# Performance work log

Hardware: AMD Instinct MI355X
Metric: run time of the kernel (lower is better)

The kernel has to match this reference:

```python
import jax, jax.numpy as jnp
import numpy as np

N_BUILDINGS = 4096
NUM_CLUSTERS = 128
EMBED_DIM = 128
TEMPORAL_DIM = 24


def setup_inputs() -> dict:
    key = jax.random.key(0)
    ks = jax.random.split(key, 12)
    E, N, C, T = EMBED_DIM, N_BUILDINGS, NUM_CLUSTERS, TEMPORAL_DIM

    def lin(k, fi, fo):
        k1, k2 = jax.random.split(k)
        w = jax.random.normal(k1, (fo, fi), jnp.float32) / np.sqrt(fi).astype(np.float32)
        b = jax.random.normal(k2, (fo,), jnp.float32) * 0.01
        return w, b

    fp_w1, fp_b1 = lin(ks[0], 2 * E + 2, 128)
    fp_w2, fp_b2 = lin(ks[1], 128, 64)
    fp_w3, fp_b3 = lin(ks[2], 64, 1)
    en_w1, en_b1 = lin(ks[3], 1, 16)
    en_w2, en_b2 = lin(ks[4], 16, 1)
    ps_w1, ps_b1 = lin(ks[5], E, 32)
    ps_w2, ps_b2 = lin(ks[6], 32, 1)

    embeddings = jax.random.normal(ks[7], (1, N, E), jnp.float32)
    generation = jax.random.uniform(ks[8], (1, N, T), jnp.float32) * 50.0
    consumption = jax.random.uniform(ks[9], (1, N, T), jnp.float32) * 50.0
    positions = jax.random.uniform(ks[10], (1, N, 2), jnp.float32) * 1000.0
    cluster_assignments = (jnp.arange(N) % C)[None, :].astype(jnp.int32)

    return dict(embeddings=embeddings, generation=generation, consumption=consumption,
                positions=positions,
                fp_w1=fp_w1, fp_b1=fp_b1, fp_w2=fp_w2, fp_b2=fp_b2, fp_w3=fp_w3, fp_b3=fp_b3,
                en_w1=en_w1, en_b1=en_b1, en_w2=en_w2, en_b2=en_b2,
                ps_w1=ps_w1, ps_b1=ps_b1, ps_w2=ps_w2, ps_b2=ps_b2,
                cluster_assignments=cluster_assignments, num_clusters=C, current_hour=12)


def _greedy_cluster(net0, prio, effm, pf):
    """Greedy allocation within one cluster. net0,prio: [K]; effm,pf: [K,K].
    Surplus rows and deficit cols are both visited in descending priority order;
    non-surplus rows have avail=0 and non-deficit cols have needed<=0, matching the
    original code's subset selection + break/continue semantics."""
    K = net0.shape[0]
    order = jnp.argsort(-prio)
    inv = jnp.argsort(order)
    net_o = net0[order]
    eff_o = effm[order][:, order]
    pf_o = pf[order][:, order]

    def outer(dnet, i):
        avail0 = jnp.maximum(net_o[i], 0.0)  # surplus net is never mutated

        def inner(carry, j):
            avail, dn = carry
            needed = -dn[j]
            active = (avail > 0.0) & (needed > 0.0)
            f = jnp.where(active, jnp.minimum(jnp.minimum(avail, needed), pf_o[i, j]), 0.0)
            dn = dn.at[j].add(f * eff_o[i, j])  # deficit receives delivered flow
            return (avail - f, dn), (f, active)

        (_, dnet), (frow, arow) = jax.lax.scan(inner, (avail0, dnet), jnp.arange(K))
        return dnet, (frow, arow)

    dnet, (flows_o, act_o) = jax.lax.scan(outer, net_o, jnp.arange(K))
    return flows_o[inv][:, inv], act_o[inv][:, inv], dnet[inv]


def _forward(embeddings, generation, consumption, positions,
             fp_w1, fp_b1, fp_w2, fp_b2, fp_w3, fp_b3,
             en_w1, en_b1, en_w2, en_b2,
             ps_w1, ps_b1, ps_w2, ps_b2,
             cluster_assignments, num_clusters, current_hour):
    B, N, E = embeddings.shape
    C = num_clusters
    K = N // C
    net = generation[0, :, current_hour] - consumption[0, :, current_hour]  # [N]

    g = jnp.argsort(cluster_assignments[0]).reshape(C, K)  # [C,K] building ids per cluster
    emb_c = embeddings[0][g]   # [C,K,E]
    pos_c = positions[0][g]    # [C,K,2]
    net_c = net[g]             # [C,K]

    # priority scorer (eval mode)
    h = jax.nn.relu(emb_c @ ps_w1.T + ps_b1)
    prio_c = jax.nn.sigmoid(h @ ps_w2.T + ps_b2)[..., 0]  # [C,K]

    # pairwise distances within cluster
    dist = jnp.linalg.norm(pos_c[:, :, None, :] - pos_c[:, None, :, :], axis=-1)  # [C,K,K]

    # efficiency net: eff = 0.85 + 0.13*sigmoid(MLP(dist/1000))
    eh = jax.nn.relu((dist / 1000.0)[..., None] * en_w1[:, 0] + en_b1)  # [C,K,K,16]
    eff = 0.85 + 0.13 * jax.nn.sigmoid(eh @ en_w2.T + en_b2)[..., 0]    # [C,K,K]

    # flow predictor on concat([emb_i, emb_j, dist, hour/24]); split W1 to avoid
    # materializing the [C,K,K,2E+2] feature tensor. Dropout is eval-mode identity.
    W1a, W1b = fp_w1[:, :E], fp_w1[:, E:2 * E]
    w1d, w1h = fp_w1[:, 2 * E], fp_w1[:, 2 * E + 1]
    hi = emb_c @ W1a.T  # [C,K,128]
    hj = emb_c @ W1b.T  # [C,K,128]
    hour_f = current_hour / 24.0
    h1 = jax.nn.relu(hi[:, :, None, :] + hj[:, None, :, :] + dist[..., None] * w1d + hour_f * w1h + fp_b1)
    h2 = jax.nn.relu(h1 @ fp_w2.T + fp_b2)
    pflow = jax.nn.softplus(h2 @ fp_w3.T + fp_b3)[..., 0]  # [C,K,K]

    flows_c, act_c, dnet_c = jax.vmap(_greedy_cluster)(net_c, prio_c, eff, pflow)

    sharing = jnp.zeros((N, N), embeddings.dtype).at[g[:, :, None], g[:, None, :]].set(flows_c)
    effmat = jnp.ones((N, N), embeddings.dtype).at[g[:, :, None], g[:, None, :]].set(
        jnp.where(act_c, eff, 1.0))
    net_after = jnp.zeros((N,), embeddings.dtype).at[g].set(dnet_c)

    sharing = sharing[None]
    effmat = effmat[None]
    total_shared = sharing.sum()
    energy_sent = sharing.sum(axis=2)
    energy_received = (sharing * effmat).sum(axis=1)
    return sharing, effmat, total_shared, energy_sent, energy_received, net_after[None]


def reference(embeddings, generation, consumption, positions,
              fp_w1, fp_b1, fp_w2, fp_b2, fp_w3, fp_b3,
              en_w1, en_b1, en_w2, en_b2,
              ps_w1, ps_b1, ps_w2, ps_b2,
              cluster_assignments, num_clusters, current_hour):
    return _forward(embeddings, generation, consumption, positions,
                    fp_w1, fp_b1, fp_w2, fp_b2, fp_w3, fp_b3,
                    en_w1, en_b1, en_w2, en_b2,
                    ps_w1, ps_b1, ps_w2, ps_b2,
                    cluster_assignments, num_clusters, current_hour)
```

## Files before the change

kernel.cpp:

```cpp
#include <hip/hip_runtime.h>
#include <math.h>

#define NB 4096
#define NC 128
#define NK 32
#define NE 128

typedef __bf16 bf16x8 __attribute__((ext_vector_type(8)));
typedef float floatx4 __attribute__((ext_vector_type(4)));

__device__ __forceinline__ float sigmoidf_(float x){
  if (x >= 0.f){ float z = expf(-x); return 1.f/(1.f+z); }
  float z = expf(x); return z/(1.f+z);
}
__device__ __forceinline__ float softplusf_(float x){
  return fmaxf(x, 0.f) + log1pf(expf(-fabsf(x)));
}
__device__ __forceinline__ unsigned int pack_bf16(float a, float b){
  unsigned short ua = __builtin_bit_cast(unsigned short, (__bf16)a);
  unsigned short ub = __builtin_bit_cast(unsigned short, (__bf16)b);
  return (unsigned int)ua | ((unsigned int)ub << 16);
}

__global__ void k_hijprio(const float* __restrict__ emb, const float* __restrict__ gen,
                          const float* __restrict__ cons, const float* __restrict__ fp_w1,
                          const float* __restrict__ fp_b1, const float* __restrict__ fp_w2,
                          const float* __restrict__ ps_w1, const float* __restrict__ ps_b1,
                          const float* __restrict__ ps_w2, const float* __restrict__ ps_b2,
                          const int* __restrict__ assign, const int* __restrict__ hourp,
                          float* __restrict__ hi, float* __restrict__ hj,
                          float* __restrict__ net, float* __restrict__ prio,
                          int* __restrict__ g, int* __restrict__ row_of,
                          float* __restrict__ w1d_c, float* __restrict__ bzc,
                          uint4* __restrict__ w2f, float* __restrict__ total){
  int bid = blockIdx.x;
  int t = threadIdx.x;
  if (bid < 512){
    __shared__ float es[8*132];
    __shared__ float wsm[32*132];
    __shared__ float wa_s[128*36];
    __shared__ float wb_s[128*36];
    int i0 = bid*8;
    for (int idx = t; idx < 8*128; idx += 256){
      int b = idx >> 7, e = idx & 127;
      es[b*132 + e] = emb[(i0 + b)*128 + e];
    }
    for (int idx = t; idx < 4096; idx += 256){
      int q = idx >> 7, e = idx & 127;
      wsm[q*132 + e] = ps_w1[q*128 + e];
    }
    int o = t & 127, half = t >> 7;
    float ai[4], aj[4];
#pragma unroll
    for (int r = 0; r < 4; ++r){ ai[r] = 0.f; aj[r] = 0.f; }
    for (int ch = 0; ch < 4; ++ch){
      int ec = ch << 5;
      if (ch) __syncthreads();
      for (int idx = t; idx < 4096; idx += 256){
        int row = idx >> 5, e2 = idx & 31;
        wa_s[row*36 + e2] = fp_w1[row*258 + ec + e2];
        wb_s[row*36 + e2] = fp_w1[row*258 + 128 + ec + e2];
      }
      __syncthreads();
      const float* war = &wa_s[o*36];
      const float* wbr = &wb_s[o*36];
#pragma unroll
      for (int e2 = 0; e2 < 32; e2 += 4){
        float4 wav = *(const float4*)&war[e2];
        float4 wbv = *(const float4*)&wbr[e2];
        float wa0 = wav.x, wa1 = wav.y, wa2 = wav.z, wa3 = wav.w;
        float wb0 = wbv.x, wb1 = wbv.y, wb2 = wbv.z, wb3 = wbv.w;
        int e = ec + e2;
#pragma unroll
        for (int r = 0; r < 4; ++r){
          float4 ev = *(const float4*)&es[(half*4 + r)*132 + e];
          ai[r] = fmaf(ev.x, wa0, fmaf(ev.y, wa1, fmaf(ev.z, wa2, fmaf(ev.w, wa3, ai[r]))));
          aj[r] = fmaf(ev.x, wb0, fmaf(ev.y, wb1, fmaf(ev.z, wb2, fmaf(ev.w, wb3, aj[r]))));
        }
      }
    }
#pragma unroll
    for (int r = 0; r < 4; ++r){
      int b = i0 + half*4 + r;
      hi[b*128 + o] = ai[r];
      hj[b*128 + o] = aj[r];
    }
    {
      int bl = t >> 5, q = t & 31;
      int i = i0 + bl;
      float acc = ps_b1[q];
      const float* er = &es[bl*132];
      const float* wr = &wsm[q*132];
      for (int e = 0; e < 128; e += 4){
        float4 ev = *(const float4*)&er[e];
        float4 wv = *(const float4*)&wr[e];
        acc = fmaf(ev.x, wv.x, acc);
        acc = fmaf(ev.y, wv.y, acc);
        acc = fmaf(ev.z, wv.z, acc);
        acc = fmaf(ev.w, wv.w, acc);
      }
      float v = fmaxf(acc, 0.f) * ps_w2[q];
      for (int m = 16; m >= 1; m >>= 1) v += __shfl_xor(v, m, 32);
      if (q == 0){
        prio[i] = sigmoidf_(v + ps_b2[0]);
        int h = hourp[0];
        net[i] = gen[i*24 + h] - cons[i*24 + h];
      }
    }
  } else if (bid < 528){
    __shared__ int hist[NC];
    __shared__ int loc[256];
    int start = (bid - 512)*256;
    for (int c = t; c < NC; c += 256) hist[c] = 0;
    __syncthreads();
    for (int j = t; j < start; j += 256) atomicAdd(&hist[assign[j]], 1);
    int i = start + t;
    int c = assign[i];
    loc[t] = c;
    __syncthreads();
    int r = hist[c];
    for (int j = 0; j < 256; ++j) r += (j < t && loc[j] == c) ? 1 : 0;
    if (r >= NK) r = NK - 1;
    g[c*NK + r] = i;
    row_of[i] = c*NK + r;
  } else if (bid == 528){
    if (t < 128){
      float hour_f = (float)hourp[0] / 24.0f;
      w1d_c[t] = fp_w1[t*258 + 256];
      bzc[t]   = fmaf(hour_f, fp_w1[t*258 + 257], fp_b1[t]);
    }
    if (t == 128) total[0] = 0.f;
  } else {
    for (int ff = t; ff < 1024; ff += 256){
      int lane = ff & 63, fi = ff >> 6;
      int nt = fi >> 2, ks = fi & 3;
      int o = nt*16 + (lane & 15);
      int kb = ks*32 + (lane >> 4)*8;
      const float* src = fp_w2 + o*128 + kb;
      uint4 u;
      u.x = pack_bf16(src[0], src[1]);
      u.y = pack_bf16(src[2], src[3]);
      u.z = pack_bf16(src[4], src[5]);
      u.w = pack_bf16(src[6], src[7]);
      w2f[ff] = u;
    }
  }
}

__global__ __launch_bounds__(512) void k_pflow(
    const float* __restrict__ hi, const float* __restrict__ hj,
    const float* __restrict__ pos, const float* __restrict__ w1d_c,
    const float* __restrict__ bzc, const uint4* __restrict__ w2f,
    const float* __restrict__ fp_b2, const float* __restrict__ fp_w3,
    const float* __restrict__ fp_b3, const float* __restrict__ en_w1,
    const float* __restrict__ en_b1, const float* __restrict__ en_w2,
    const float* __restrict__ en_b2, const int* __restrict__ g,
    float* __restrict__ pf_g, float* __restrict__ ef_g){
  __shared__ float px[32], py[32];
  __shared__ int gl[32];
  int t = threadIdx.x;
  int lane = t & 63, wv = t >> 6;
  int c = blockIdx.x >> 1, hb = blockIdx.x & 1;
  if (t < 32){
    int b = g[c*NK + t];
    gl[t] = b;
    px[t] = pos[2*b];
    py[t] = pos[2*b + 1];
  }
  __syncthreads();
  {
    int l16 = lane & 15, quad = lane >> 4;
    bf16x8 bfr[4][4];
#pragma unroll
    for (int nt = 0; nt < 4; ++nt)
#pragma unroll
      for (int ks = 0; ks < 4; ++ks)
        bfr[nt][ks] = __builtin_bit_cast(bf16x8, w2f[(nt*4 + ks)*64 + lane]);
    float b2v[4], w3v[4];
#pragma unroll
    for (int nt = 0; nt < 4; ++nt){
      b2v[nt] = fp_b2[nt*16 + l16];
      w3v[nt] = fp_w3[nt*16 + l16];
    }
    float b3 = fp_b3[0];
    const float4* wd4 = (const float4*)w1d_c;
    const float4* bz4 = (const float4*)bzc;
    for (int it = 0; it < 4; ++it){
      int tile = hb*32 + it*8 + wv;
      int i = tile >> 1, j0 = (tile & 1)*16;
      int j = j0 + l16;
      float dx = px[i] - px[j], dy = py[i] - py[j];
      float d = sqrtf(fmaf(dx, dx, dy*dy));
      const float4* hi4 = (const float4*)(hi + gl[i]*128);
      const float4* hj4 = (const float4*)(hj + gl[j]*128);
      bf16x8 af[4];
#pragma unroll
      for (int ks = 0; ks < 4; ++ks){
        int q8 = ks*8 + quad*2;
        float4 a0 = hi4[q8], a1 = hi4[q8 + 1];
        float4 b0 = hj4[q8], b1 = hj4[q8 + 1];
        float4 w0 = wd4[q8], w1 = wd4[q8 + 1];
        float4 z0 = bz4[q8], z1 = bz4[q8 + 1];
        float v0 = fmaxf(a0.x + b0.x + fmaf(d, w0.x, z0.x), 0.f);
        float v1 = fmaxf(a0.y + b0.y + fmaf(d, w0.y, z0.y), 0.f);
        float v2 = fmaxf(a0.z + b0.z + fmaf(d, w0.z, z0.z), 0.f);
        float v3 = fmaxf(a0.w + b0.w + fmaf(d, w0.w, z0.w), 0.f);
        float v4 = fmaxf(a1.x + b1.x + fmaf(d, w1.x, z1.x), 0.f);
        float v5 = fmaxf(a1.y + b1.y + fmaf(d, w1.y, z1.y), 0.f);
        float v6 = fmaxf(a1.z + b1.z + fmaf(d, w1.z, z1.z), 0.f);
        float v7 = fmaxf(a1.w + b1.w + fmaf(d, w1.w, z1.w), 0.f);
        uint4 u;
        u.x = pack_bf16(v0, v1);
        u.y = pack_bf16(v2, v3);
        u.z = pack_bf16(v4, v5);
        u.w = pack_bf16(v6, v7);
        af[ks] = __builtin_bit_cast(bf16x8, u);
      }
      floatx4 acc[4];
#pragma unroll
      for (int nt = 0; nt < 4; ++nt){
        acc[nt] = (floatx4){0.f, 0.f, 0.f, 0.f};
#pragma unroll
        for (int ks = 0; ks < 4; ++ks)
          acc[nt] = __builtin_amdgcn_mfma_f32_16x16x32_bf16(af[ks], bfr[nt][ks], acc[nt], 0, 0, 0);
      }
#pragma unroll
      for (int r = 0; r < 4; ++r){
        float s = 0.f;
#pragma unroll
        for (int nt = 0; nt < 4; ++nt)
          s = fmaf(fmaxf(acc[nt][r] + b2v[nt], 0.f), w3v[nt], s);
#pragma unroll
        for (int m = 8; m >= 1; m >>= 1) s += __shfl_xor(s, m);
        if (l16 == 0)
          pf_g[c*1024 + i*32 + j0 + quad*4 + r] = softplusf_(s + b3);
      }
    }
  }
  {
    int e = hb*512 + t;
    int ii = e >> 5, jj = e & 31;
    float dx = px[ii] - px[jj], dy = py[ii] - py[jj];
    float d = sqrtf(fmaf(dx, dx, dy*dy));
    float ds = d * (1.0f/1000.0f);
    float acc = en_b2[0];
#pragma unroll
    for (int q = 0; q < 16; ++q)
      acc = fmaf(fmaxf(fmaf(ds, en_w1[q], en_b1[q]), 0.f), en_w2[q], acc);
    ef_g[c*1024 + e] = 0.85f + 0.13f*sigmoidf_(acc);
  }
}

__global__ __launch_bounds__(256) void k_gw(
    const float* __restrict__ net, const float* __restrict__ prio,
    const int* __restrict__ g, const float* __restrict__ pf_g,
    const float* __restrict__ ef_g, float* __restrict__ total,
    float* __restrict__ esent, float* __restrict__ erecv, float* __restrict__ nafter,
    float* __restrict__ sharing, float* __restrict__ effm){
  __shared__ float pf_s[1024];
  __shared__ float ef_s[1024];
  __shared__ float fl_s[1024];
  __shared__ float efa_s[1024];
  __shared__ int   mtbl[NB];
  __shared__ int   gl[32];
  __shared__ int   order_s[32];
  int t = threadIdx.x;
  int c = blockIdx.x >> 1, hb = blockIdx.x & 1;
  if (t < 32) gl[t] = g[c*NK + t];
  ((float4*)pf_s)[t] = ((const float4*)(pf_g + c*1024))[t];
  ((float4*)ef_s)[t] = ((const float4*)(ef_g + c*1024))[t];
#pragma unroll
  for (int q = 0; q < 16; ++q) mtbl[q*256 + t] = -1;
  __syncthreads();
  if (t < 32) mtbl[gl[t]] = t;
  if (t < 64){
    int tl = t & 31;
    float pr = (t < 32) ? prio[gl[t]] : -1e30f;
    int rank = 0;
    for (int k = 0; k < 32; ++k){
      float pk = __shfl(pr, k, 32);
      rank += ((pk > pr) || (pk == pr && k < tl)) ? 1 : 0;
    }
    if (t < 32) order_s[rank] = t;
  }
  __syncthreads();
  if (t < 64){
    int tl = t & 31;
    int b = order_s[tl];
    float net0 = net[gl[b]];
    float dnet = net0;
    float recv = 0.f;
    for (int i = 0; i < 32; ++i){
      int a = order_s[i];
      float av0 = fmaxf(__shfl(net0, i, 32), 0.f);
      float pf = pf_s[a*32 + b];
      float ef = ef_s[a*32 + b];
      float needed = -dnet;
      float m = (needed > 0.f) ? fminf(needed, pf) : 0.f;
      float s = m;
#pragma unroll
      for (int dd = 1; dd < 32; dd <<= 1){
        float u = __shfl_up(s, dd, 32);
        if (tl >= dd) s += u;
      }
      float Se = __shfl_up(s, 1, 32);
      if (tl == 0) Se = 0.f;
      float rprev = fmaxf(av0 - Se, 0.f);
      int act = (rprev > 0.f) && (needed > 0.f);
      float f = fminf(m, rprev);
      dnet = fmaf(f, ef, dnet);
      recv = fmaf(f, ef, recv);
      if (t < 32){
        fl_s[a*32 + b]  = f;
        efa_s[a*32 + b] = act ? ef : 1.0f;
      }
    }
    if (hb == 0 && t < 32){
      nafter[gl[b]] = dnet;
      erecv[gl[b]]  = recv;
    }
  }
  __syncthreads();
  if (hb == 0 && t < 32){
    float rs = 0.f;
#pragma unroll
    for (int j = 0; j < 32; ++j)
      rs += fl_s[t*32 + ((j + t) & 31)];
    esent[gl[t]] = rs;
    float cs = rs;
    for (int m = 16; m >= 1; m >>= 1) cs += __shfl_xor(cs, m, 32);
    if (t == 0) atomicAdd(total, cs);
  }
  int mjq[16];
#pragma unroll
  for (int q = 0; q < 4; ++q)
#pragma unroll
    for (int x = 0; x < 4; ++x)
      mjq[q*4 + x] = mtbl[q*1024 + t*4 + x];
  for (int al = 0; al < 16; ++al){
    int a = hb*16 + al;
    long row = (long)gl[a] * NB;
    const float* flr = &fl_s[a*32];
    const float* efr = &efa_s[a*32];
    floatx4* gs = (floatx4*)(sharing + row);
    floatx4* ge = (floatx4*)(effm + row);
#pragma unroll
    for (int q = 0; q < 4; ++q){
      floatx4 vs = (floatx4){0.f, 0.f, 0.f, 0.f};
      floatx4 ve = (floatx4){1.f, 1.f, 1.f, 1.f};
#pragma unroll
      for (int x = 0; x < 4; ++x){
        int mj = mjq[q*4 + x];
        if (mj >= 0){ vs[x] = flr[mj]; ve[x] = efr[mj]; }
      }
      __builtin_nontemporal_store(vs, &gs[q*256 + t]);
      __builtin_nontemporal_store(ve, &ge[q*256 + t]);
    }
  }
}

extern "C" void kernel_launch(void* const* d_in, const int* in_sizes, int n_in,
                              void* d_out, int out_size, void* d_ws, size_t ws_size,
                              hipStream_t stream){
  (void)in_sizes; (void)n_in; (void)out_size; (void)ws_size;
  const float* emb   = (const float*)d_in[0];
  const float* gen   = (const float*)d_in[1];
  const float* cons  = (const float*)d_in[2];
  const float* pos   = (const float*)d_in[3];
  const float* fp_w1 = (const float*)d_in[4];
  const float* fp_b1 = (const float*)d_in[5];
  const float* fp_w2 = (const float*)d_in[6];
  const float* fp_b2 = (const float*)d_in[7];
  const float* fp_w3 = (const float*)d_in[8];
  const float* fp_b3 = (const float*)d_in[9];
  const float* en_w1 = (const float*)d_in[10];
  const float* en_b1 = (const float*)d_in[11];
  const float* en_w2 = (const float*)d_in[12];
  const float* en_b2 = (const float*)d_in[13];
  const float* ps_w1 = (const float*)d_in[14];
  const float* ps_b1 = (const float*)d_in[15];
  const float* ps_w2 = (const float*)d_in[16];
  const float* ps_b2 = (const float*)d_in[17];
  const int*   assign = (const int*)d_in[18];
  const int*   hourp  = (const int*)d_in[20];

  char* ws = (char*)d_ws;
  int*   g      = (int*)  (ws + 0);
  int*   row_of = (int*)  (ws + 16384);
  float* net    = (float*)(ws + 32768);
  float* prio   = (float*)(ws + 49152);
  float* w1d_c  = (float*)(ws + 65536);
  float* bzc    = (float*)(ws + 66048);
  uint4* w2f    = (uint4*)(ws + 131072);
  float* hi     = (float*)(ws + 262144);
  float* hj     = (float*)(ws + 2359296);
  float* pf_g   = (float*)(ws + 5505024);
  float* ef_g   = (float*)(ws + 6029312);

  float* sharing = (float*)d_out;
  float* effm    = sharing + (long)NB*NB;
  float* total   = effm + (long)NB*NB;
  float* esent   = total + 1;
  float* erecv   = esent + NB;
  float* nafter  = erecv + NB;

  hipLaunchKernelGGL(k_hijprio, dim3(530), dim3(256), 0, stream,
                     emb, gen, cons, fp_w1, fp_b1, fp_w2, ps_w1, ps_b1, ps_w2, ps_b2,
                     assign, hourp, hi, hj, net, prio, g, row_of, w1d_c, bzc, w2f, total);
  hipLaunchKernelGGL(k_pflow, dim3(256), dim3(512), 0, stream,
                     hi, hj, pos, w1d_c, bzc, w2f, fp_b2, fp_w3, fp_b3,
                     en_w1, en_b1, en_w2, en_b2, g, pf_g, ef_g);
  hipLaunchKernelGGL(k_gw, dim3(256), dim3(256), 0, stream,
                     net, prio, g, pf_g, ef_g, total, esent, erecv, nafter,
                     sharing, effm);
}
```

Measured before the change: 241.3 us.

## Fuse three kernels into one cooperative kernel with grid syncs

Merges the prep (hi/hj/prio/grouping), pairwise-flow MLP, and greedy/write kernels into a single cooperative launch of 256 blocks of 512 threads, separated by grid.sync calls. Block work is re-partitioned: each block now handles 16 buildings in the first phase, and the final write loop stripes over 512 threads. This removes two kernel launch boundaries and their gaps. In exchange it adds grid-wide barrier cost and a larger combined shared-memory footprint per block, which may lower occupancy. The big output write (two 4096x4096 float matrices) still dominates.

```diff
diff --git a/kernel.cpp b/kernel.cpp
--- a/kernel.cpp
+++ b/kernel.cpp
@@ -1,5 +1,8 @@
 #include <hip/hip_runtime.h>
+#include <hip/hip_cooperative_groups.h>
 #include <math.h>
+
+namespace cg = cooperative_groups;
 
 #define NB 4096
 #define NC 128
@@ -22,30 +25,50 @@
   return (unsigned int)ua | ((unsigned int)ub << 16);
 }
 
-__global__ void k_hijprio(const float* __restrict__ emb, const float* __restrict__ gen,
-                          const float* __restrict__ cons, const float* __restrict__ fp_w1,
-                          const float* __restrict__ fp_b1, const float* __restrict__ fp_w2,
-                          const float* __restrict__ ps_w1, const float* __restrict__ ps_b1,
-                          const float* __restrict__ ps_w2, const float* __restrict__ ps_b2,
-                          const int* __restrict__ assign, const int* __restrict__ hourp,
-                          float* __restrict__ hi, float* __restrict__ hj,
-                          float* __restrict__ net, float* __restrict__ prio,
-                          int* __restrict__ g, int* __restrict__ row_of,
-                          float* __restrict__ w1d_c, float* __restrict__ bzc,
-                          uint4* __restrict__ w2f, float* __restrict__ total){
+__global__ __launch_bounds__(512) void k_fused(
+    const float* __restrict__ emb, const float* __restrict__ gen,
+    const float* __restrict__ cons, const float* __restrict__ pos,
+    const float* __restrict__ fp_w1, const float* __restrict__ fp_b1,
+    const float* __restrict__ fp_w2, const float* __restrict__ fp_b2,
+    const float* __restrict__ fp_w3, const float* __restrict__ fp_b3,
+    const float* __restrict__ en_w1, const float* __restrict__ en_b1,
+    const float* __restrict__ en_w2, const float* __restrict__ en_b2,
+    const float* __restrict__ ps_w1, const float* __restrict__ ps_b1,
+    const float* __restrict__ ps_w2, const float* __restrict__ ps_b2,
+    const int* __restrict__ assign, const int* __restrict__ hourp,
+    int* __restrict__ g, float* __restrict__ net, float* __restrict__ prio,
+    float* __restrict__ w1d_c, float* __restrict__ bzc, uint4* __restrict__ w2f,
+    float* __restrict__ hi, float* __restrict__ hj,
+    float* __restrict__ pf_g, float* __restrict__ ef_g,
+    float* __restrict__ total, float* __restrict__ esent,
+    float* __restrict__ erecv, float* __restrict__ nafter,
+    float* __restrict__ sharing, float* __restrict__ effm){
+  cg::grid_group grid = cg::this_grid();
   int bid = blockIdx.x;
   int t = threadIdx.x;
-  if (bid < 512){
-    __shared__ float es[8*132];
-    __shared__ float wsm[32*132];
-    __shared__ float wa_s[128*36];
-    __shared__ float wb_s[128*36];
-    int i0 = bid*8;
-    for (int idx = t; idx < 8*128; idx += 256){
+
+  __shared__ float es[16*132];
+  __shared__ float wsm[32*132];
+  __shared__ float wa_s[128*36];
+  __shared__ float wb_s[128*36];
+  __shared__ int   hist[NC];
+  __shared__ int   loc[256];
+  __shared__ float px[32], py[32];
+  __shared__ int   gl[32];
+  __shared__ float pf_s[1024];
+  __shared__ float ef_s[1024];
+  __shared__ float fl_s[1024];
+  __shared__ float efa_s[1024];
+  __shared__ int   mtbl[NB];
+  __shared__ int   order_s[32];
+
+  {
+    int i0 = bid*16;
+    for (int idx = t; idx < 16*128; idx += 512){
       int b = idx >> 7, e = idx & 127;
       es[b*132 + e] = emb[(i0 + b)*128 + e];
     }
-    for (int idx = t; idx < 4096; idx += 256){
+    for (int idx = t; idx < 4096; idx += 512){
       int q = idx >> 7, e = idx & 127;
       wsm[q*132 + e] = ps_w1[q*128 + e];
     }
@@ -56,7 +79,7 @@
     for (int ch = 0; ch < 4; ++ch){
       int ec = ch << 5;
       if (ch) __syncthreads();
-      for (int idx = t; idx < 4096; idx += 256){
+      for (int idx = t; idx < 4096; idx += 512){
         int row = idx >> 5, e2 = idx & 31;
         wa_s[row*36 + e2] = fp_w1[row*258 + ec + e2];
         wb_s[row*36 + e2] = fp_w1[row*258 + 128 + ec + e2];
@@ -107,60 +130,48 @@
         net[i] = gen[i*24 + h] - cons[i*24 + h];
       }
     }
-  } else if (bid < 528){
-    __shared__ int hist[NC];
-    __shared__ int loc[256];
-    int start = (bid - 512)*256;
-    for (int c = t; c < NC; c += 256) hist[c] = 0;
-    __syncthreads();
-    for (int j = t; j < start; j += 256) atomicAdd(&hist[assign[j]], 1);
-    int i = start + t;
-    int c = assign[i];
-    loc[t] = c;
-    __syncthreads();
-    int r = hist[c];
-    for (int j = 0; j < 256; ++j) r += (j < t && loc[j] == c) ? 1 : 0;
-    if (r >= NK) r = NK - 1;
-    g[c*NK + r] = i;
-    row_of[i] = c*NK + r;
-  } else if (bid == 528){
-    if (t < 128){
-      float hour_f = (float)hourp[0] / 24.0f;
-      w1d_c[t] = fp_w1[t*258 + 256];
-      bzc[t]   = fmaf(hour_f, fp_w1[t*258 + 257], fp_b1[t]);
-    }
-    if (t == 128) total[0] = 0.f;
-  } else {
-    for (int ff = t; ff < 1024; ff += 256){
-      int lane = ff & 63, fi = ff >> 6;
-      int nt = fi >> 2, ks = fi & 3;
-      int o = nt*16 + (lane & 15);
-      int kb = ks*32 + (lane >> 4)*8;
-      const float* src = fp_w2 + o*128 + kb;
-      uint4 u;
-      u.x = pack_bf16(src[0], src[1]);
-      u.y = pack_bf16(src[2], src[3]);
-      u.z = pack_bf16(src[4], src[5]);
-      u.w = pack_bf16(src[6], src[7]);
-      w2f[ff] = u;
-    }
-  }
-}
-
-__global__ __launch_bounds__(512) void k_pflow(
-    const float* __restrict__ hi, const float* __restrict__ hj,
-    const float* __restrict__ pos, const float* __restrict__ w1d_c,
-    const float* __restrict__ bzc, const uint4* __restrict__ w2f,
-    const float* __restrict__ fp_b2, const float* __restrict__ fp_w3,
-    const float* __restrict__ fp_b3, const float* __restrict__ en_w1,
-    const float* __restrict__ en_b1, const float* __restrict__ en_w2,
-    const float* __restrict__ en_b2, const int* __restrict__ g,
-    float* __restrict__ pf_g, float* __restrict__ ef_g){
-  __shared__ float px[32], py[32];
-  __shared__ int gl[32];
-  int t = threadIdx.x;
+    if (bid < 16){
+      int start = bid*256;
+      for (int c2 = t; c2 < NC; c2 += 512) hist[c2] = 0;
+      __syncthreads();
+      for (int j = t; j < start; j += 512) atomicAdd(&hist[assign[j]], 1);
+      if (t < 256) loc[t] = assign[start + t];
+      __syncthreads();
+      if (t < 256){
+        int i = start + t;
+        int c2 = loc[t];
+        int r = hist[c2];
+        for (int j = 0; j < 256; ++j) r += (j < t && loc[j] == c2) ? 1 : 0;
+        if (r >= NK) r = NK - 1;
+        g[c2*NK + r] = i;
+      }
+    } else if (bid == 16){
+      if (t < 128){
+        float hour_f = (float)hourp[0] / 24.0f;
+        w1d_c[t] = fp_w1[t*258 + 256];
+        bzc[t]   = fmaf(hour_f, fp_w1[t*258 + 257], fp_b1[t]);
+      }
+      if (t == 128) total[0] = 0.f;
+    } else if (bid == 17){
+      for (int ff = t; ff < 1024; ff += 512){
+        int lane2 = ff & 63, fi = ff >> 6;
+        int nt = fi >> 2, ks = fi & 3;
+        int oo = nt*16 + (lane2 & 15);
+        int kb = ks*32 + (lane2 >> 4)*8;
+        const float* src = fp_w2 + oo*128 + kb;
+        uint4 u;
+        u.x = pack_bf16(src[0], src[1]);
+        u.y = pack_bf16(src[2], src[3]);
+        u.z = pack_bf16(src[4], src[5]);
+        u.w = pack_bf16(src[6], src[7]);
+        w2f[ff] = u;
+      }
+    }
+  }
+  grid.sync();
+
   int lane = t & 63, wv = t >> 6;
-  int c = blockIdx.x >> 1, hb = blockIdx.x & 1;
+  int c = bid >> 1, hb = bid & 1;
   if (t < 32){
     int b = g[c*NK + t];
     gl[t] = b;
@@ -249,28 +260,14 @@
       acc = fmaf(fmaxf(fmaf(ds, en_w1[q], en_b1[q]), 0.f), en_w2[q], acc);
     ef_g[c*1024 + e] = 0.85f + 0.13f*sigmoidf_(acc);
   }
-}
-
-__global__ __launch_bounds__(256) void k_gw(
-    const float* __restrict__ net, const float* __restrict__ prio,
-    const int* __restrict__ g, const float* __restrict__ pf_g,
-    const float* __restrict__ ef_g, float* __restrict__ total,
-    float* __restrict__ esent, float* __restrict__ erecv, float* __restrict__ nafter,
-    float* __restrict__ sharing, float* __restrict__ effm){
-  __shared__ float pf_s[1024];
-  __shared__ float ef_s[1024];
-  __shared__ float fl_s[1024];
-  __shared__ float efa_s[1024];
-  __shared__ int   mtbl[NB];
-  __shared__ int   gl[32];
-  __shared__ int   order_s[32];
-  int t = threadIdx.x;
-  int c = blockIdx.x >> 1, hb = blockIdx.x & 1;
-  if (t < 32) gl[t] = g[c*NK + t];
-  ((float4*)pf_s)[t] = ((const float4*)(pf_g + c*1024))[t];
-  ((float4*)ef_s)[t] = ((const float4*)(ef_g + c*1024))[t];
-#pragma unroll
-  for (int q = 0; q < 16; ++q) mtbl[q*256 + t] = -1;
+  grid.sync();
+
+  if (t < 256){
+    ((float4*)pf_s)[t] = ((const float4*)(pf_g + c*1024))[t];
+    ((float4*)ef_s)[t] = ((const float4*)(ef_g + c*1024))[t];
+  }
+#pragma unroll
+  for (int q = 0; q < 8; ++q) mtbl[q*512 + t] = -1;
   __syncthreads();
   if (t < 32) mtbl[gl[t]] = t;
   if (t < 64){
@@ -331,12 +328,12 @@
     for (int m = 16; m >= 1; m >>= 1) cs += __shfl_xor(cs, m, 32);
     if (t == 0) atomicAdd(total, cs);
   }
-  int mjq[16];
-#pragma unroll
-  for (int q = 0; q < 4; ++q)
+  int mjq[8];
+#pragma unroll
+  for (int q = 0; q < 2; ++q)
 #pragma unroll
     for (int x = 0; x < 4; ++x)
-      mjq[q*4 + x] = mtbl[q*1024 + t*4 + x];
+      mjq[q*4 + x] = mtbl[q*2048 + t*4 + x];
   for (int al = 0; al < 16; ++al){
     int a = hb*16 + al;
     long row = (long)gl[a] * NB;
@@ -345,7 +342,7 @@
     floatx4* gs = (floatx4*)(sharing + row);
     floatx4* ge = (floatx4*)(effm + row);
 #pragma unroll
-    for (int q = 0; q < 4; ++q){
+    for (int q = 0; q < 2; ++q){
       floatx4 vs = (floatx4){0.f, 0.f, 0.f, 0.f};
       floatx4 ve = (floatx4){1.f, 1.f, 1.f, 1.f};
 #pragma unroll
@@ -353,8 +350,8 @@
         int mj = mjq[q*4 + x];
         if (mj >= 0){ vs[x] = flr[mj]; ve[x] = efr[mj]; }
       }
-      __builtin_nontemporal_store(vs, &gs[q*256 + t]);
-      __builtin_nontemporal_store(ve, &ge[q*256 + t]);
+      __builtin_nontemporal_store(vs, &gs[q*512 + t]);
+      __builtin_nontemporal_store(ve, &ge[q*512 + t]);
     }
   }
 }
@@ -386,7 +383,6 @@
 
   char* ws = (char*)d_ws;
   int*   g      = (int*)  (ws + 0);
-  int*   row_of = (int*)  (ws + 16384);
   float* net    = (float*)(ws + 32768);
   float* prio   = (float*)(ws + 49152);
   float* w1d_c  = (float*)(ws + 65536);
@@ -404,13 +400,17 @@
   float* erecv   = esent + NB;
   float* nafter  = erecv + NB;
 
-  hipLaunchKernelGGL(k_hijprio, dim3(530), dim3(256), 0, stream,
-                     emb, gen, cons, fp_w1, fp_b1, fp_w2, ps_w1, ps_b1, ps_w2, ps_b2,
-                     assign, hourp, hi, hj, net, prio, g, row_of, w1d_c, bzc, w2f, total);
-  hipLaunchKernelGGL(k_pflow, dim3(256), dim3(512), 0, stream,
-                     hi, hj, pos, w1d_c, bzc, w2f, fp_b2, fp_w3, fp_b3,
-                     en_w1, en_b1, en_w2, en_b2, g, pf_g, ef_g);
-  hipLaunchKernelGGL(k_gw, dim3(256), dim3(256), 0, stream,
-                     net, prio, g, pf_g, ef_g, total, esent, erecv, nafter,
-                     sharing, effm);
+  void* args[] = {
+    (void*)&emb, (void*)&gen, (void*)&cons, (void*)&pos,
+    (void*)&fp_w1, (void*)&fp_b1, (void*)&fp_w2, (void*)&fp_b2,
+    (void*)&fp_w3, (void*)&fp_b3, (void*)&en_w1, (void*)&en_b1,
+    (void*)&en_w2, (void*)&en_b2, (void*)&ps_w1, (void*)&ps_b1,
+    (void*)&ps_w2, (void*)&ps_b2, (void*)&assign, (void*)&hourp,
+    (void*)&g, (void*)&net, (void*)&prio, (void*)&w1d_c, (void*)&bzc,
+    (void*)&w2f, (void*)&hi, (void*)&hj, (void*)&pf_g, (void*)&ef_g,
+    (void*)&total, (void*)&esent, (void*)&erecv, (void*)&nafter,
+    (void*)&sharing, (void*)&effm
+  };
+  hipLaunchCooperativeKernel((const void*)k_fused, dim3(256), dim3(512),
+                             args, 0, stream);
 }
```

After: 313.3 us. +29.9%, slower.

## Fuse pair-flow MLP and greedy/write kernels into one per-cluster kernel

Applied to the files above, without the earlier changes.

Merges the pair-flow MLP kernel and the greedy allocation plus scatter-write kernel into a single launch, keeping pf and ef tables in shared memory instead of a global round-trip. Each of the two blocks per cluster now computes the full 32x32 pair-flow MLP redundantly so that both halves have the complete table, and the 512-thread block then writes half the rows. This removes one launch and the global intermediate buffers, at the cost of doubling the MLP work and larger shared memory per block.

```diff
diff --git a/kernel.cpp b/kernel.cpp
--- a/kernel.cpp
+++ b/kernel.cpp
@@ -147,17 +147,26 @@
   }
 }
 
-__global__ __launch_bounds__(512) void k_pflow(
+__global__ __launch_bounds__(512) void k_pfgw(
     const float* __restrict__ hi, const float* __restrict__ hj,
-    const float* __restrict__ pos, const float* __restrict__ w1d_c,
+    const float* __restrict__ pos, const float* __restrict__ net,
+    const float* __restrict__ prio, const float* __restrict__ w1d_c,
     const float* __restrict__ bzc, const uint4* __restrict__ w2f,
     const float* __restrict__ fp_b2, const float* __restrict__ fp_w3,
     const float* __restrict__ fp_b3, const float* __restrict__ en_w1,
     const float* __restrict__ en_b1, const float* __restrict__ en_w2,
     const float* __restrict__ en_b2, const int* __restrict__ g,
-    float* __restrict__ pf_g, float* __restrict__ ef_g){
+    float* __restrict__ total, float* __restrict__ esent,
+    float* __restrict__ erecv, float* __restrict__ nafter,
+    float* __restrict__ sharing, float* __restrict__ effm){
+  __shared__ float pf_s[1024];
+  __shared__ float ef_s[1024];
+  __shared__ float fl_s[1024];
+  __shared__ float efa_s[1024];
   __shared__ float px[32], py[32];
-  __shared__ int gl[32];
+  __shared__ int   gl[32];
+  __shared__ int   order_s[32];
+  __shared__ int   mtbl[NB];
   int t = threadIdx.x;
   int lane = t & 63, wv = t >> 6;
   int c = blockIdx.x >> 1, hb = blockIdx.x & 1;
@@ -167,7 +176,10 @@
     px[t] = pos[2*b];
     py[t] = pos[2*b + 1];
   }
+#pragma unroll
+  for (int q = 0; q < 8; ++q) mtbl[q*512 + t] = -1;
   __syncthreads();
+  if (t < 32) mtbl[gl[t]] = t;
   {
     int l16 = lane & 15, quad = lane >> 4;
     bf16x8 bfr[4][4];
@@ -185,8 +197,8 @@
     float b3 = fp_b3[0];
     const float4* wd4 = (const float4*)w1d_c;
     const float4* bz4 = (const float4*)bzc;
-    for (int it = 0; it < 4; ++it){
-      int tile = hb*32 + it*8 + wv;
+    for (int it = 0; it < 8; ++it){
+      int tile = it*8 + wv;
       int i = tile >> 1, j0 = (tile & 1)*16;
       int j = j0 + l16;
       float dx = px[i] - px[j], dy = py[i] - py[j];
@@ -233,12 +245,11 @@
 #pragma unroll
         for (int m = 8; m >= 1; m >>= 1) s += __shfl_xor(s, m);
         if (l16 == 0)
-          pf_g[c*1024 + i*32 + j0 + quad*4 + r] = softplusf_(s + b3);
-      }
-    }
-  }
-  {
-    int e = hb*512 + t;
+          pf_s[i*32 + j0 + quad*4 + r] = softplusf_(s + b3);
+      }
+    }
+  }
+  for (int e = t; e < 1024; e += 512){
     int ii = e >> 5, jj = e & 31;
     float dx = px[ii] - px[jj], dy = py[ii] - py[jj];
     float d = sqrtf(fmaf(dx, dx, dy*dy));
@@ -247,32 +258,8 @@
 #pragma unroll
     for (int q = 0; q < 16; ++q)
       acc = fmaf(fmaxf(fmaf(ds, en_w1[q], en_b1[q]), 0.f), en_w2[q], acc);
-    ef_g[c*1024 + e] = 0.85f + 0.13f*sigmoidf_(acc);
-  }
-}
-
-__global__ __launch_bounds__(256) void k_gw(
-    const float* __restrict__ net, const float* __restrict__ prio,
-    const int* __restrict__ g, const float* __restrict__ pf_g,
-    const float* __restrict__ ef_g, float* __restrict__ total,
-    float* __restrict__ esent, float* __restrict__ erecv, float* __restrict__ nafter,
-    float* __restrict__ sharing, float* __restrict__ effm){
-  __shared__ float pf_s[1024];
-  __shared__ float ef_s[1024];
-  __shared__ float fl_s[1024];
-  __shared__ float efa_s[1024];
-  __shared__ int   mtbl[NB];
-  __shared__ int   gl[32];
-  __shared__ int   order_s[32];
-  int t = threadIdx.x;
-  int c = blockIdx.x >> 1, hb = blockIdx.x & 1;
-  if (t < 32) gl[t] = g[c*NK + t];
-  ((float4*)pf_s)[t] = ((const float4*)(pf_g + c*1024))[t];
-  ((float4*)ef_s)[t] = ((const float4*)(ef_g + c*1024))[t];
-#pragma unroll
-  for (int q = 0; q < 16; ++q) mtbl[q*256 + t] = -1;
-  __syncthreads();
-  if (t < 32) mtbl[gl[t]] = t;
+    ef_s[e] = 0.85f + 0.13f*sigmoidf_(acc);
+  }
   if (t < 64){
     int tl = t & 31;
     float pr = (t < 32) ? prio[gl[t]] : -1e30f;
@@ -331,12 +318,12 @@
     for (int m = 16; m >= 1; m >>= 1) cs += __shfl_xor(cs, m, 32);
     if (t == 0) atomicAdd(total, cs);
   }
-  int mjq[16];
-#pragma unroll
-  for (int q = 0; q < 4; ++q)
+  int mjq[8];
+#pragma unroll
+  for (int q = 0; q < 2; ++q)
 #pragma unroll
     for (int x = 0; x < 4; ++x)
-      mjq[q*4 + x] = mtbl[q*1024 + t*4 + x];
+      mjq[q*4 + x] = mtbl[q*2048 + t*4 + x];
   for (int al = 0; al < 16; ++al){
     int a = hb*16 + al;
     long row = (long)gl[a] * NB;
@@ -345,7 +332,7 @@
     floatx4* gs = (floatx4*)(sharing + row);
     floatx4* ge = (floatx4*)(effm + row);
 #pragma unroll
-    for (int q = 0; q < 4; ++q){
+    for (int q = 0; q < 2; ++q){
       floatx4 vs = (floatx4){0.f, 0.f, 0.f, 0.f};
       floatx4 ve = (floatx4){1.f, 1.f, 1.f, 1.f};
 #pragma unroll
@@ -353,8 +340,8 @@
         int mj = mjq[q*4 + x];
         if (mj >= 0){ vs[x] = flr[mj]; ve[x] = efr[mj]; }
       }
-      __builtin_nontemporal_store(vs, &gs[q*256 + t]);
-      __builtin_nontemporal_store(ve, &ge[q*256 + t]);
+      __builtin_nontemporal_store(vs, &gs[q*512 + t]);
+      __builtin_nontemporal_store(ve, &ge[q*512 + t]);
     }
   }
 }
@@ -394,8 +381,6 @@
   uint4* w2f    = (uint4*)(ws + 131072);
   float* hi     = (float*)(ws + 262144);
   float* hj     = (float*)(ws + 2359296);
-  float* pf_g   = (float*)(ws + 5505024);
-  float* ef_g   = (float*)(ws + 6029312);
 
   float* sharing = (float*)d_out;
   float* effm    = sharing + (long)NB*NB;
@@ -407,10 +392,8 @@
   hipLaunchKernelGGL(k_hijprio, dim3(530), dim3(256), 0, stream,
                      emb, gen, cons, fp_w1, fp_b1, fp_w2, ps_w1, ps_b1, ps_w2, ps_b2,
                      assign, hourp, hi, hj, net, prio, g, row_of, w1d_c, bzc, w2f, total);
-  hipLaunchKernelGGL(k_pflow, dim3(256), dim3(512), 0, stream,
-                     hi, hj, pos, w1d_c, bzc, w2f, fp_b2, fp_w3, fp_b3,
-                     en_w1, en_b1, en_w2, en_b2, g, pf_g, ef_g);
-  hipLaunchKernelGGL(k_gw, dim3(256), dim3(256), 0, stream,
-                     net, prio, g, pf_g, ef_g, total, esent, erecv, nafter,
-                     sharing, effm);
-}
+  hipLaunchKernelGGL(k_pfgw, dim3(256), dim3(512), 0, stream,
+                     hi, hj, pos, net, prio, w1d_c, bzc, w2f, fp_b2, fp_w3, fp_b3,
+                     en_w1, en_b1, en_w2, en_b2, g,
+                     total, esent, erecv, nafter, sharing, effm);
+}
```

New measurement: 252.9 us. 4.8% more time.
